# Kernel tuning notes

Measured on AMD Instinct MI355X. Metric: run time of the kernel, lower is better.

## Reference

```python
import jax, jax.numpy as jnp
import numpy as np

B, T, F, H, P = 4, 1024, 500, 128, 64


def setup_inputs() -> dict:
    key = jax.random.key(0)
    ks = jax.random.split(key, 10)
    s_gru = 1.0 / np.sqrt(H)
    s_ctx = 1.0 / np.sqrt(2 * H * P)
    s_fc = 1.0 / np.sqrt(H)
    return {
        "x": jax.random.normal(ks[0], (B, T, F), dtype=jnp.float32),
        "W_ih": jax.random.uniform(ks[1], (3 * H, F), jnp.float32, -s_gru, s_gru),
        "W_hh": jax.random.uniform(ks[2], (3 * H, H), jnp.float32, -s_gru, s_gru),
        "b_ih": jax.random.uniform(ks[3], (3 * H,), jnp.float32, -s_gru, s_gru),
        "b_hh": jax.random.uniform(ks[4], (3 * H,), jnp.float32, -s_gru, s_gru),
        "W_ctx": jax.random.uniform(ks[5], (H, 2 * H * P), jnp.float32, -s_ctx, s_ctx),
        "b_ctx": jax.random.uniform(ks[6], (H,), jnp.float32, -s_ctx, s_ctx),
        "W_fc": jax.random.uniform(ks[7], (P, H), jnp.float32, -s_fc, s_fc),
        "b_fc": jax.random.uniform(ks[8], (P,), jnp.float32, -s_fc, s_fc),
    }


def reference(x, W_ih, W_hh, b_ih, b_hh, W_ctx, b_ctx, W_fc, b_fc):
    # Original torch code never updates `hidden` inside the time loop, so every
    # GRU step runs with h = 0 (W_hh contributes only through b_hh). For a
    # 1-layer GRU, output == new state. PyTorch gate order: r, z, n.
    Bv, Tv, _ = x.shape
    Hv = W_hh.shape[1]
    Pv = W_fc.shape[0]
    gi = jnp.einsum('btf,gf->btg', x, W_ih) + b_ih          # [B,T,3H]
    gr, gz, gn = jnp.split(gi, 3, axis=-1)
    br, bz, bn = jnp.split(b_hh, 3)
    r = jax.nn.sigmoid(gr + br)
    z = jax.nn.sigmoid(gz + bz)
    n = jnp.tanh(gn + r * bn)                               # W_hh @ 0 == 0
    states = (1.0 - z) * n                                  # [B,T,H], h' = (1-z)*n + z*0
    all_states = jnp.transpose(states, (1, 0, 2))           # [T,B,H]

    # context_mat[:, :, j] at step i = concat(state_i, state_{max(i-j,0)})
    idx = jnp.clip(jnp.arange(Tv)[:, None] - jnp.arange(Pv)[None, :], 0)  # [T,P]
    gathered = all_states[idx]                              # [T,P,B,H]
    part1 = jnp.broadcast_to(all_states[:, :, :, None], (Tv, Bv, Hv, Pv))
    part2 = jnp.transpose(gathered, (0, 2, 3, 1))           # [T,B,H,P]
    # flatten matches torch .view(B, -1) of [B, 2H, P]: channel-major then proposal
    ctx_in = jnp.concatenate([part1, part2], axis=2).reshape(Tv, Bv, 2 * Hv * Pv)
    gate = jax.nn.sigmoid(jnp.einsum('tbc,hc->tbh', ctx_in, W_ctx) + b_ctx)
    gated = all_states * gate                               # output_i * ctx gate

    outs = jnp.transpose(gated, (1, 0, 2))                  # [B,T,H]
    probs = jax.nn.sigmoid(jnp.einsum('bth,ph->btp', outs, W_fc) + b_fc)
    probs = jnp.clip(probs, 0.001, 0.999)                   # [B,T,P]
    return probs, all_states
```

## Files before the change

### kernel.cpp

```cpp
#include <hip/hip_runtime.h>


typedef short bf16x8 __attribute__((ext_vector_type(8)));
typedef float f32x4 __attribute__((ext_vector_type(4)));
typedef unsigned short u16;
typedef unsigned int u32;

__device__ __forceinline__ float bf2f(u16 u) {
  union { u32 i; float f; } v; v.i = ((u32)u) << 16; return v.f;
}
__device__ __forceinline__ u16 f2bf(float f) {
  union { float f; u32 i; } v; v.f = f;
  u32 u = v.i;
  return (u16)((u + 0x7FFFu + ((u >> 16) & 1u)) >> 16);
}
__device__ __forceinline__ u32 pack2(float a, float b) {
  return (u32)f2bf(a) | ((u32)f2bf(b) << 16);
}
__device__ __forceinline__ float sigmoidf_(float x) {
  return 1.0f / (1.0f + __expf(-x));
}

__global__ __launch_bounds__(256) void k_prep(const float* __restrict__ W_ctx,
                                              u16* __restrict__ Wc) {
  const int tid = threadIdx.x;
  __shared__ float t1[128][68];
  __shared__ float t2[128][68];
  __shared__ float s1[128];
  const int hp = blockIdx.x;
  const float* wrow = W_ctx + hp * 16384;
  for (int it = 0; it < 8; ++it) {
    int i = it * 256 + tid;
    int j = i * 4;
    int h = j >> 6, q = j & 63;
    *(float4*)&t1[h][q] = *(const float4*)(wrow + j);
    *(float4*)&t2[h][q] = *(const float4*)(wrow + 8192 + j);
  }
  __syncthreads();
  if (tid < 128) {
    float s = 0.f;
    for (int q = 0; q < 64; ++q) s += t1[tid][q];
    s1[tid] = s;
  }
  __syncthreads();
  for (int it = 0; it < 8; ++it) {
    int i = it * 256 + tid;
    int p = i >> 5, h0 = (i & 31) * 4;
    float v0 = t2[h0 + 0][p], v1 = t2[h0 + 1][p];
    float v2 = t2[h0 + 2][p], v3 = t2[h0 + 3][p];
    if (p == 0) { v0 += s1[h0]; v1 += s1[h0 + 1]; v2 += s1[h0 + 2]; v3 += s1[h0 + 3]; }
    uint2 o; o.x = pack2(v0, v1); o.y = pack2(v2, v3);
    *(uint2*)(Wc + p * 16384 + hp * 128 + h0) = o;
  }
}

__global__ __launch_bounds__(512, 4) void k_gemm_gi(const float* __restrict__ x,
                                                    const float* __restrict__ W_ih,
                                                    u16* __restrict__ gi_bf) {
  __shared__ u16 Asm[2][64][64];
  __shared__ u16 Bsm[2][128][64];
  const int tid = threadIdx.x;
  const int w = tid >> 6, lane = tid & 63;
  const int l15 = lane & 15, quad = lane >> 4;
  const int wm = (w & 1) * 32, wn = (w >> 1) * 32;
  const int m0 = blockIdx.x * 64;
  const int n0 = blockIdx.y * 128;
  f32x4 acc[2][2];
  for (int i = 0; i < 2; ++i)
    for (int j = 0; j < 2; ++j) acc[i][j] = (f32x4){0.f, 0.f, 0.f, 0.f};

  uint4 ra, rb[2];
  auto cvt_load = [](const float* base, int k) -> uint4 {
    float4 a = make_float4(0.f, 0.f, 0.f, 0.f), b = a;
    if (k < 500)     a = *(const float4*)(base + k);
    if (k + 4 < 500) b = *(const float4*)(base + k + 4);
    uint4 o; o.x = pack2(a.x, a.y); o.y = pack2(a.z, a.w);
    o.z = pack2(b.x, b.y); o.w = pack2(b.z, b.w);
    return o;
  };
  auto load_step = [&](int s) {
    int kc = s * 64;
    {
      int c = tid;
      ra = cvt_load(x + (size_t)(m0 + (c >> 3)) * 500, kc + (c & 7) * 8);
    }
#pragma unroll
    for (int j = 0; j < 2; ++j) {
      int c = j * 512 + tid;
      rb[j] = cvt_load(W_ih + (size_t)(n0 + (c >> 3)) * 500, kc + (c & 7) * 8);
    }
  };
  auto write_step = [&](int b) {
    {
      int c = tid;
      int r = c >> 3, pc = (c & 7) ^ (r & 7);
      *(uint4*)&Asm[b][r][pc * 8] = ra;
    }
#pragma unroll
    for (int j = 0; j < 2; ++j) {
      int c = j * 512 + tid;
      int r = c >> 3, pc = (c & 7) ^ (r & 7);
      *(uint4*)&Bsm[b][r][pc * 8] = rb[j];
    }
  };

  load_step(0); write_step(0); __syncthreads();
  for (int s = 0; s < 8; ++s) {
    int cur = s & 1;
    if (s < 7) load_step(s + 1);
#pragma unroll
    for (int kk = 0; kk < 2; ++kk) {
      int ch = kk * 4 + quad;
      bf16x8 af[2], bfr[2];
#pragma unroll
      for (int mt = 0; mt < 2; ++mt) {
        int r = wm + mt * 16 + l15;
        af[mt] = *(const bf16x8*)&Asm[cur][r][(ch ^ (r & 7)) * 8];
      }
#pragma unroll
      for (int nt = 0; nt < 2; ++nt) {
        int r = wn + nt * 16 + l15;
        bfr[nt] = *(const bf16x8*)&Bsm[cur][r][(ch ^ (r & 7)) * 8];
      }
#pragma unroll
      for (int mt = 0; mt < 2; ++mt)
#pragma unroll
        for (int nt = 0; nt < 2; ++nt)
          acc[mt][nt] = __builtin_amdgcn_mfma_f32_16x16x32_bf16(af[mt], bfr[nt], acc[mt][nt], 0, 0, 0);
    }
    if (s < 7) write_step((s + 1) & 1);
    __syncthreads();
  }
  for (int mt = 0; mt < 2; ++mt)
    for (int nt = 0; nt < 2; ++nt)
      for (int rg = 0; rg < 4; ++rg) {
        int m = m0 + wm + mt * 16 + quad * 4 + rg;
        int n = n0 + wn + nt * 16 + l15;
        gi_bf[m * 384 + n] = f2bf(acc[mt][nt][rg]);
      }
}

__global__ void k_states(const u16* __restrict__ gi_bf,
                         const float* __restrict__ b_ih, const float* __restrict__ b_hh,
                         u16* __restrict__ S_bf, float* __restrict__ out_states) {
  int g = blockIdx.x * 256 + threadIdx.x;
  int r = g >> 7, h = g & 127;
  float xr = bf2f(gi_bf[r * 384 + h])       + b_ih[h]       + b_hh[h];
  float xz = bf2f(gi_bf[r * 384 + 128 + h]) + b_ih[128 + h] + b_hh[128 + h];
  float xn = bf2f(gi_bf[r * 384 + 256 + h]) + b_ih[256 + h];
  float rg = sigmoidf_(xr);
  float zg = sigmoidf_(xz);
  float n = tanhf(xn + rg * b_hh[256 + h]);
  float s = (1.f - zg) * n;
  int b = r >> 10, t = r & 1023;
  S_bf[(t * 4 + b) * 128 + h] = f2bf(s);
  out_states[(t * 4 + b) * 128 + h] = s;
}

__global__ __launch_bounds__(512, 6) void k_gemm_ctx(const u16* __restrict__ S_bf,
                                                     const u16* __restrict__ Wc,
                                                     float* __restrict__ partial) {
  __shared__ u16 Awin[92][128];
  const int tid = threadIdx.x;
  const int w = tid >> 6, lane = tid & 63;
  const int l15 = lane & 15, quad = lane >> 4;
  const int wm = (w & 1) * 32, wn = (w >> 1) * 16;
  const int m0 = blockIdx.x * 64;
  const int n0 = blockIdx.y * 64;
  const int P0 = blockIdx.z * 8;
  const int tlo = (m0 >> 2) - P0 - 7;
  f32x4 acc[2];
  acc[0] = (f32x4){0.f, 0.f, 0.f, 0.f};
  acc[1] = (f32x4){0.f, 0.f, 0.f, 0.f};

  for (int it = 0; it < 3; ++it) {
    int idx = it * 512 + tid;
    if (idx < 1472) {
      int r = idx >> 4, ch = idx & 15;
      int t = tlo + (r >> 2); if (t < 0) t = 0;
      uint4 v = *(const uint4*)(S_bf + (size_t)(t * 4 + (r & 3)) * 128 + ch * 8);
      *(uint4*)&Awin[r][(((ch & 7) ^ (r & 7)) | (ch & 8)) * 8] = v;
    }
  }
  __syncthreads();

  const u16* wbase = Wc + (size_t)P0 * 16384
                        + (size_t)(n0 + wn + l15) * 128 + quad * 8;
#pragma unroll
  for (int p = 0; p < 8; ++p) {
    const int shift = 4 * (7 - p);
    const u16* wp = wbase + (size_t)p * 16384;
    bf16x8 bfr[4];
#pragma unroll
    for (int kk = 0; kk < 4; ++kk)
      bfr[kk] = *(const bf16x8*)(wp + kk * 32);
#pragma unroll
    for (int kk = 0; kk < 4; ++kk) {
      const int ach = kk * 4 + quad;
      bf16x8 af[2];
#pragma unroll
      for (int mt = 0; mt < 2; ++mt) {
        int r = wm + mt * 16 + l15 + shift;
        af[mt] = *(const bf16x8*)&Awin[r][(((ach & 7) ^ (r & 7)) | (ach & 8)) * 8];
      }
#pragma unroll
      for (int mt = 0; mt < 2; ++mt)
        acc[mt] = __builtin_amdgcn_mfma_f32_16x16x32_bf16(af[mt], bfr[kk], acc[mt], 0, 0, 0);
    }
  }
  float* op = partial + (size_t)blockIdx.z * 524288;
#pragma unroll
  for (int mt = 0; mt < 2; ++mt)
#pragma unroll
    for (int rg = 0; rg < 4; ++rg) {
      int m = m0 + wm + mt * 16 + quad * 4 + rg;
      int n = n0 + wn + l15;
      op[m * 128 + n] = acc[mt][rg];
    }
}

__global__ __launch_bounds__(256) void k_epilogue(const float* __restrict__ partial,
                                                  const float* __restrict__ states,
                                                  const float* __restrict__ b_ctx,
                                                  const float* __restrict__ W_fc,
                                                  const float* __restrict__ b_fc,
                                                  float* __restrict__ out_probs) {
  __shared__ float WfcT[128][68];
  __shared__ float gated[8][128];
  const int tid = threadIdx.x;
  const int row0 = blockIdx.x * 8;
  for (int it = 0; it < 32; ++it) {
    int i = it * 256 + tid;
    int pp = i >> 7, h = i & 127;
    WfcT[h][pp] = W_fc[i];
  }
  for (int it = 0; it < 4; ++it) {
    int i = it * 256 + tid;
    int lr = i >> 7, h = i & 127;
    int sr = row0 + lr;
    float gp = b_ctx[h];
#pragma unroll
    for (int c = 0; c < 8; ++c) gp += partial[(size_t)c * 524288 + sr * 128 + h];
    gated[lr][h] = states[sr * 128 + h] * sigmoidf_(gp);
  }
  __syncthreads();
  for (int it = 0; it < 2; ++it) {
    int o = it * 256 + tid;
    int lr = o >> 6, pp = o & 63;
    int sr = row0 + lr;
    float dot = 0.f;
#pragma unroll
    for (int h = 0; h < 128; ++h) dot += gated[lr][h] * WfcT[h][pp];
    float pv = sigmoidf_(dot + b_fc[pp]);
    pv = (pv > 0.001f) ? pv : 0.001f;
    pv = (pv < 0.999f) ? pv : 0.999f;
    int t = sr >> 2, b = sr & 3;
    out_probs[(b * 1024 + t) * 64 + pp] = pv;
  }
}

extern "C" void kernel_launch(void* const* d_in, const int* in_sizes, int n_in,
                              void* d_out, int out_size, void* d_ws, size_t ws_size,
                              hipStream_t stream) {
  const float* x     = (const float*)d_in[0];
  const float* W_ih  = (const float*)d_in[1];
  const float* b_ih  = (const float*)d_in[3];
  const float* b_hh  = (const float*)d_in[4];
  const float* W_ctx = (const float*)d_in[5];
  const float* b_ctx = (const float*)d_in[6];
  const float* W_fc  = (const float*)d_in[7];
  const float* b_fc  = (const float*)d_in[8];
  float* out = (float*)d_out;

  char* ws = (char*)d_ws;
  u16*   gi_bf   = (u16*)  (ws + 0);
  u16*   S_bf    = (u16*)  (ws + 3145728);
  u16*   Wc      = (u16*)  (ws + 4194304);
  float* partial = (float*)(ws + 6291456);

  k_prep<<<128, 256, 0, stream>>>(W_ctx, Wc);
  k_gemm_gi<<<dim3(64, 3), 512, 0, stream>>>(x, W_ih, gi_bf);
  k_states<<<2048, 256, 0, stream>>>(gi_bf, b_ih, b_hh, S_bf, out + 262144);
  k_gemm_ctx<<<dim3(64, 2, 8), 512, 0, stream>>>(S_bf, Wc, partial);
  k_epilogue<<<512, 256, 0, stream>>>(partial, out + 262144, b_ctx, W_fc, b_fc, out);
}
```

Baseline: 133.6 us.

## Switch ctx GEMM to 32x32 MFMA with pre-tiled weight layout; vectorize epilogue

The context GEMM now uses 32x32x16 bf16 MFMA, with each block covering all 128 output columns instead of splitting N over two blocks. The packed context weights are re-laid out in k_prep into 8-element K-chunk tiles so that B-fragment loads are contiguous. This halves the redundant staging of the shared-memory A window and launches fewer blocks with larger per-wave tiles, at some cost in occupancy. The epilogue loads W_fc with float4 into an XOR-swizzled shared array and computes the dot product with vectorized reads.

```diff
diff --git a/kernel.cpp b/kernel.cpp
--- a/kernel.cpp
+++ b/kernel.cpp
@@ -3,6 +3,7 @@
 
 typedef short bf16x8 __attribute__((ext_vector_type(8)));
 typedef float f32x4 __attribute__((ext_vector_type(4)));
+typedef float f32x16 __attribute__((ext_vector_type(16)));
 typedef unsigned short u16;
 typedef unsigned int u32;
 
@@ -22,7 +23,7 @@
 }
 
 __global__ __launch_bounds__(256) void k_prep(const float* __restrict__ W_ctx,
-                                              u16* __restrict__ Wc) {
+                                              u16* __restrict__ WcT) {
   const int tid = threadIdx.x;
   __shared__ float t1[128][68];
   __shared__ float t2[128][68];
@@ -50,7 +51,7 @@
     float v2 = t2[h0 + 2][p], v3 = t2[h0 + 3][p];
     if (p == 0) { v0 += s1[h0]; v1 += s1[h0 + 1]; v2 += s1[h0 + 2]; v3 += s1[h0 + 3]; }
     uint2 o; o.x = pack2(v0, v1); o.y = pack2(v2, v3);
-    *(uint2*)(Wc + p * 16384 + hp * 128 + h0) = o;
+    *(uint2*)(WcT + ((size_t)(p * 16 + (h0 >> 3)) * 128 + hp) * 8 + (h0 & 7)) = o;
   }
 }
 
@@ -157,65 +158,60 @@
   out_states[(t * 4 + b) * 128 + h] = s;
 }
 
-__global__ __launch_bounds__(512, 6) void k_gemm_ctx(const u16* __restrict__ S_bf,
-                                                     const u16* __restrict__ Wc,
+__global__ __launch_bounds__(256, 2) void k_gemm_ctx(const u16* __restrict__ S_bf,
+                                                     const u16* __restrict__ WcT,
                                                      float* __restrict__ partial) {
   __shared__ u16 Awin[92][128];
   const int tid = threadIdx.x;
   const int w = tid >> 6, lane = tid & 63;
-  const int l15 = lane & 15, quad = lane >> 4;
-  const int wm = (w & 1) * 32, wn = (w >> 1) * 16;
+  const int l31 = lane & 31, half = lane >> 5;
+  const int wm = (w & 1) * 32;
+  const int wn = (w >> 1) * 64;
   const int m0 = blockIdx.x * 64;
-  const int n0 = blockIdx.y * 64;
-  const int P0 = blockIdx.z * 8;
+  const int P0 = blockIdx.y * 8;
   const int tlo = (m0 >> 2) - P0 - 7;
-  f32x4 acc[2];
-  acc[0] = (f32x4){0.f, 0.f, 0.f, 0.f};
-  acc[1] = (f32x4){0.f, 0.f, 0.f, 0.f};
-
-  for (int it = 0; it < 3; ++it) {
-    int idx = it * 512 + tid;
+  f32x16 acc[2];
+#pragma unroll
+  for (int i = 0; i < 16; ++i) { acc[0][i] = 0.f; acc[1][i] = 0.f; }
+
+  for (int it = 0; it < 6; ++it) {
+    int idx = it * 256 + tid;
     if (idx < 1472) {
       int r = idx >> 4, ch = idx & 15;
       int t = tlo + (r >> 2); if (t < 0) t = 0;
       uint4 v = *(const uint4*)(S_bf + (size_t)(t * 4 + (r & 3)) * 128 + ch * 8);
-      *(uint4*)&Awin[r][(((ch & 7) ^ (r & 7)) | (ch & 8)) * 8] = v;
-    }
-  }
-  __syncthreads();
-
-  const u16* wbase = Wc + (size_t)P0 * 16384
-                        + (size_t)(n0 + wn + l15) * 128 + quad * 8;
-#pragma unroll
-  for (int p = 0; p < 8; ++p) {
-    const int shift = 4 * (7 - p);
-    const u16* wp = wbase + (size_t)p * 16384;
-    bf16x8 bfr[4];
-#pragma unroll
-    for (int kk = 0; kk < 4; ++kk)
-      bfr[kk] = *(const bf16x8*)(wp + kk * 32);
-#pragma unroll
-    for (int kk = 0; kk < 4; ++kk) {
-      const int ach = kk * 4 + quad;
-      bf16x8 af[2];
-#pragma unroll
-      for (int mt = 0; mt < 2; ++mt) {
-        int r = wm + mt * 16 + l15 + shift;
-        af[mt] = *(const bf16x8*)&Awin[r][(((ach & 7) ^ (r & 7)) | (ach & 8)) * 8];
-      }
-#pragma unroll
-      for (int mt = 0; mt < 2; ++mt)
-        acc[mt] = __builtin_amdgcn_mfma_f32_16x16x32_bf16(af[mt], bfr[kk], acc[mt], 0, 0, 0);
-    }
-  }
-  float* op = partial + (size_t)blockIdx.z * 524288;
-#pragma unroll
-  for (int mt = 0; mt < 2; ++mt)
-#pragma unroll
-    for (int rg = 0; rg < 4; ++rg) {
-      int m = m0 + wm + mt * 16 + quad * 4 + rg;
-      int n = n0 + wn + l15;
-      op[m * 128 + n] = acc[mt][rg];
+      *(uint4*)&Awin[r][((ch ^ (r & 15)) & 15) * 8] = v;
+    }
+  }
+  __syncthreads();
+
+  const u16* wbase = WcT + (size_t)half * 1024 + (size_t)(wn + l31) * 8;
+#pragma unroll
+  for (int pi = 0; pi < 8; ++pi) {
+    const int shift = 4 * (7 - pi);
+    const size_t pofs = (size_t)((P0 + pi) * 16) * 1024;
+#pragma unroll
+    for (int ks = 0; ks < 8; ++ks) {
+      bf16x8 bfr[2];
+#pragma unroll
+      for (int nt = 0; nt < 2; ++nt)
+        bfr[nt] = *(const bf16x8*)(wbase + pofs + (size_t)(ks * 2) * 1024 + nt * 256);
+      int r = wm + shift + l31;
+      int kc = ks * 2 + half;
+      bf16x8 af = *(const bf16x8*)&Awin[r][((kc ^ (r & 15)) & 15) * 8];
+#pragma unroll
+      for (int nt = 0; nt < 2; ++nt)
+        acc[nt] = __builtin_amdgcn_mfma_f32_32x32x16_bf16(af, bfr[nt], acc[nt], 0, 0, 0);
+    }
+  }
+  float* op = partial + (size_t)blockIdx.y * 524288;
+#pragma unroll
+  for (int nt = 0; nt < 2; ++nt)
+#pragma unroll
+    for (int rg = 0; rg < 16; ++rg) {
+      int m = m0 + wm + (rg & 3) + 8 * (rg >> 2) + 4 * half;
+      int n = wn + nt * 32 + l31;
+      op[m * 128 + n] = acc[nt][rg];
     }
 }
 
@@ -225,14 +221,15 @@
                                                   const float* __restrict__ W_fc,
                                                   const float* __restrict__ b_fc,
                                                   float* __restrict__ out_probs) {
-  __shared__ float WfcT[128][68];
+  __shared__ float Wfc2[64][128];
   __shared__ float gated[8][128];
   const int tid = threadIdx.x;
   const int row0 = blockIdx.x * 8;
-  for (int it = 0; it < 32; ++it) {
-    int i = it * 256 + tid;
-    int pp = i >> 7, h = i & 127;
-    WfcT[h][pp] = W_fc[i];
+  for (int it = 0; it < 8; ++it) {
+    int i = it * 256 + tid;
+    int pp = i >> 5, c = i & 31;
+    float4 v = *(const float4*)(W_fc + i * 4);
+    *(float4*)&Wfc2[pp][((c ^ pp) & 31) * 4] = v;
   }
   for (int it = 0; it < 4; ++it) {
     int i = it * 256 + tid;
@@ -250,7 +247,11 @@
     int sr = row0 + lr;
     float dot = 0.f;
 #pragma unroll
-    for (int h = 0; h < 128; ++h) dot += gated[lr][h] * WfcT[h][pp];
+    for (int i = 0; i < 32; ++i) {
+      float4 g = *(const float4*)&gated[lr][i * 4];
+      float4 wv = *(const float4*)&Wfc2[pp][((i ^ pp) & 31) * 4];
+      dot += g.x * wv.x + g.y * wv.y + g.z * wv.z + g.w * wv.w;
+    }
     float pv = sigmoidf_(dot + b_fc[pp]);
     pv = (pv > 0.001f) ? pv : 0.001f;
     pv = (pv < 0.999f) ? pv : 0.999f;
@@ -275,12 +276,12 @@
   char* ws = (char*)d_ws;
   u16*   gi_bf   = (u16*)  (ws + 0);
   u16*   S_bf    = (u16*)  (ws + 3145728);
-  u16*   Wc      = (u16*)  (ws + 4194304);
+  u16*   WcT     = (u16*)  (ws + 4194304);
   float* partial = (float*)(ws + 6291456);
 
-  k_prep<<<128, 256, 0, stream>>>(W_ctx, Wc);
+  k_prep<<<128, 256, 0, stream>>>(W_ctx, WcT);
   k_gemm_gi<<<dim3(64, 3), 512, 0, stream>>>(x, W_ih, gi_bf);
   k_states<<<2048, 256, 0, stream>>>(gi_bf, b_ih, b_hh, S_bf, out + 262144);
-  k_gemm_ctx<<<dim3(64, 2, 8), 512, 0, stream>>>(S_bf, Wc, partial);
+  k_gemm_ctx<<<dim3(64, 8), 256, 0, stream>>>(S_bf, WcT, partial);
   k_epilogue<<<512, 256, 0, stream>>>(partial, out + 262144, b_ctx, W_fc, b_fc, out);
 }
```

Measured after the change: 124.4 us. -6.9%, faster.
